# Kernel optimization log

Measured on AMD Instinct MI355X. Metric: run time of the kernel, lower is better.

The kernel has to match this reference:

```python
import jax, jax.numpy as jnp
import numpy as np

FORGET_BIAS = 1.0  # tf.nn.rnn_cell.LSTMCell default


def _lstm_scan(x_btE, W, b, hidden):
    """x: (B,T,E). W: (E+H, 4H), gate order i, j, f, o (TF LSTMCell)."""
    B = x_btE.shape[0]
    h0 = jnp.zeros((B, hidden), x_btE.dtype)
    c0 = jnp.zeros((B, hidden), x_btE.dtype)

    def step(carry, x_t):
        h, c = carry
        z = jnp.concatenate([x_t, h], axis=-1) @ W + b  # (B, 4H)
        i, j, f, o = jnp.split(z, 4, axis=-1)
        c_new = jax.nn.sigmoid(f + FORGET_BIAS) * c + jax.nn.sigmoid(i) * jnp.tanh(j)
        h_new = jax.nn.sigmoid(o) * jnp.tanh(c_new)
        return (h_new, c_new), h_new

    (_, _), hs = jax.lax.scan(step, (h0, c0), jnp.swapaxes(x_btE, 0, 1))
    return jnp.swapaxes(hs, 0, 1)  # (B, T, H)


def setup_inputs() -> dict:
    key = jax.random.key(0)
    ks = jax.random.split(key, 5)
    B, T, V, E, H, C = 256, 120, 50000, 256, 1024, 5
    tokens = jax.random.randint(ks[0], (B, T, 1), 0, V, dtype=jnp.int32)
    embeddings = jax.random.normal(ks[1], (V, E), jnp.float32) * 0.1
    W_lstm = jax.random.normal(ks[2], (E + H, 4 * H), jnp.float32) * (1.0 / np.sqrt(E + H))
    b_lstm = jnp.zeros((4 * H,), jnp.float32)
    U = jax.random.normal(ks[3], (H, C), jnp.float32) * (1.0 / np.sqrt(H))
    b2 = jnp.zeros((C,), jnp.float32)
    return {"tokens": tokens, "embeddings": embeddings, "W_lstm": W_lstm,
            "b_lstm": b_lstm, "U": U, "b2": b2}


def reference(tokens, embeddings, W_lstm, b_lstm, U, b2):
    B, T, F = tokens.shape  # F == n_features == 1
    E = embeddings.shape[1]
    H = U.shape[0]
    # embedding lookup + reshape to (B, T, F*E)
    x = embeddings[tokens].reshape(B, T, F * E)
    outputs = _lstm_scan(x, W_lstm, b_lstm, H)  # (B, T, H); dropout keep_prob=1 -> identity
    preds = outputs.reshape(-1, H) @ U + b2
    return preds.reshape(B, T, -1)  # (B, max_length, n_classes)
```

## Files before the change

### kernel.cpp

```cpp
#include <hip/hip_runtime.h>

typedef unsigned short u16;
typedef unsigned int u32;
typedef unsigned long long u64;
typedef int   v4i  __attribute__((ext_vector_type(4)));
typedef short v8s  __attribute__((ext_vector_type(8)));
typedef float v2f  __attribute__((ext_vector_type(2)));
typedef float v16f __attribute__((ext_vector_type(16)));

#define B_ 256
#define T_ 120
#define E_ 256
#define H_ 1024
#define K_ 1280
#define LDH 1032
#define LDX 264

#define WS_WF   0
#define WS_X    10485760
#define WS_HS   26214400
#define WS_BAR  89128960

__device__ __forceinline__ u16 f2bf(float f) {
    union { float f; u32 u; } v; v.f = f;
    u32 r = v.u + 0x7fffu + ((v.u >> 16) & 1u);
    return (u16)(r >> 16);
}
__device__ __forceinline__ float bf2f(u16 u) {
    union { u32 u; float f; } v; v.u = ((u32)u) << 16; return v.f;
}
__device__ __forceinline__ float fsig(float x) {
    float t = __builtin_amdgcn_exp2f(-1.44269504f * x);
    return __builtin_amdgcn_rcpf(1.0f + t);
}
__device__ __forceinline__ float ftanh_(float x) {
    float xc = fminf(8.0f, fmaxf(-8.0f, x));
    float t = __builtin_amdgcn_exp2f(2.88539008f * xc);
    return (t - 1.0f) * __builtin_amdgcn_rcpf(t + 1.0f);
}
__device__ __forceinline__ void gl_lds16(const void* g, void* l) {
    __builtin_amdgcn_global_load_lds(
        (const __attribute__((address_space(1))) void*)g,
        (__attribute__((address_space(3))) void*)l, 16, 0, 0);
}

__global__ void prep_all(const float* __restrict__ W, u16* __restrict__ Wf,
                         const int* __restrict__ tokens, const float* __restrict__ emb,
                         u16* __restrict__ X) {
    __shared__ u16 tile[64 * 72];
    int bid = blockIdx.x;
    int tid = threadIdx.x;
    if (bid < 1280) {
        int cid = bid / 5, fo = bid % 5;
        int kq  = cid & 3, np = (cid >> 2) & 1, nc = cid >> 3;
        int cc = tid & 31, n = (tid >> 5) & 1, r = tid >> 6;
        int col = (np * 2 + n) * 1024 + nc * 32 + cc;
#pragma unroll
        for (int fl = 0; fl < 4; ++fl) {
            int k0 = (4 * (fo * 4 + fl) + kq) * 16;
#pragma unroll
            for (int rr = 0; rr < 4; ++rr) {
                int krow = rr * 4 + r;
                float v = W[(size_t)(k0 + krow) * 4096 + col];
                tile[(n * 32 + cc) * 72 + fl * 16 + krow] = f2bf(v);
            }
        }
        __syncthreads();
        int lane = tid & 63, wvv = tid >> 6;
#pragma unroll
        for (int pass = 0; pass < 2; ++pass) {
            int slot = wvv + pass * 4;
            int fl = slot >> 1, nn = slot & 1;
            v4i o = *(const v4i*)&tile[(nn * 32 + (lane & 31)) * 72 + fl * 16 + ((lane >> 5) << 3)];
            *(v4i*)(Wf + (size_t)cid * 20480 + (((fo * 4 + fl) * 2 + nn) << 9) + lane * 8) = o;
        }
    } else {
        int v   = (bid - 1280) * 256 + tid;
        int e8  = v & 31;
        int row = v >> 5;
        int t = row >> 8, b = row & 255;
        int tok = tokens[b * T_ + t];
        const float* src = emb + (size_t)tok * E_ + e8 * 8;
        u16 o[8];
#pragma unroll
        for (int j = 0; j < 8; ++j) o[j] = f2bf(src[j]);
        *(v4i*)(X + (size_t)row * E_ + e8 * 8) = *(v4i*)o;
    }
}

__global__ __launch_bounds__(512, 2) void lstm_main(
    const u16* __restrict__ Wf, const u16* __restrict__ X,
    const float* __restrict__ b_lstm, u16* __restrict__ hs,
    u32* __restrict__ bar) {

    __shared__ u16  hbuf[32 * LDH];
    __shared__ u16  xbuf[32 * LDX];
    __shared__ float gates[4 * 4 * 32 * 34];
    __shared__ float bias[128];

    const int tid   = threadIdx.x;
    const int lane  = tid & 63;
    const int wv    = tid >> 6;
    const int np    = wv >> 2;
    const int kq    = wv & 3;
    const int bid   = blockIdx.x;
    const int mchunk = bid & 7;
    const int nc    = bid >> 3;
    const int m0    = mchunk << 5;

    if (tid < 128) bias[tid] = b_lstm[(tid >> 5) * H_ + (nc << 5) + (tid & 31)];

    v8s Wr[20][2];
    {
        const v4i* wsrc = (const v4i*)(Wf + (size_t)(nc * 8 + np * 4 + kq) * 20480);
#pragma unroll
        for (int f = 0; f < 20; ++f)
#pragma unroll
            for (int n = 0; n < 2; ++n)
                Wr[f][n] = __builtin_bit_cast(v8s, wsrc[(f * 2 + n) * 64 + lane]);
    }
#pragma unroll
    for (int f = 0; f < 20; ++f) {
        asm volatile("" : "+v"(Wr[f][0]));
        asm volatile("" : "+v"(Wr[f][1]));
    }

    {
        const v4i* xs = (const v4i*)(X + (size_t)m0 * E_);
#pragma unroll
        for (int i = 0; i < 2; ++i) {
            int idx = tid + i * 512;
            int r = idx >> 5, c8 = idx & 31;
            *(v4i*)&xbuf[r * LDX + c8 * 8] = xs[r * 32 + c8];
        }
    }
    __syncthreads();

    const u16* Ax = &xbuf[(lane & 31) * LDX + ((lane >> 5) << 3)];
    const u16* Ah = &hbuf[(lane & 31) * LDH + ((lane >> 5) << 3)];

    v16f acc0 = {0,0,0,0,0,0,0,0,0,0,0,0,0,0,0,0};
    v16f acc1 = {0,0,0,0,0,0,0,0,0,0,0,0,0,0,0,0};
#pragma unroll
    for (int f = 0; f < 4; ++f) {
        v8s a = *(const v8s*)(Ax + (4 * f + kq) * 16);
        acc0 = __builtin_amdgcn_mfma_f32_32x32x16_bf16(a, Wr[f][0], acc0, 0, 0, 0);
        acc1 = __builtin_amdgcn_mfma_f32_32x32x16_bf16(a, Wr[f][1], acc1, 0, 0, 0);
    }

    float cst[2] = {0.f, 0.f};
    const int cm  = tid >> 4;
    const int cn2 = (tid & 15) << 1;
    u32* hs32 = (u32*)hs;

    for (int t = 0; t < T_; ++t) {
        if (t > 0) {
            if (tid == 0) {
                u32* p = &bar[((size_t)(mchunk * T_ + (t - 1))) << 4];
                while (__hip_atomic_load(p, __ATOMIC_RELAXED, __HIP_MEMORY_SCOPE_AGENT) < 32u)
                    __builtin_amdgcn_s_sleep(1);
            }
            __syncthreads();
            {
                const u16* srcb = hs + ((size_t)(t - 1) * B_ + m0) * H_;
                const int r0 = wv << 2;
#pragma unroll
                for (int i = 0; i < 4; ++i)
                    gl_lds16(srcb + (size_t)(r0 + i) * H_ + lane * 8,
                             &hbuf[(r0 + i) * LDH]);
#pragma unroll
                for (int i = 0; i < 4; ++i)
                    gl_lds16(srcb + (size_t)(r0 + i) * H_ + 512 + lane * 8,
                             &hbuf[(r0 + i) * LDH + 512]);
            }
            asm volatile("s_waitcnt vmcnt(4)\n\ts_barrier" ::: "memory");
#pragma unroll
            for (int f = 4; f < 12; ++f) {
                v8s a = *(const v8s*)(Ah + (4 * f + kq) * 16 - 256);
                acc0 = __builtin_amdgcn_mfma_f32_32x32x16_bf16(a, Wr[f][0], acc0, 0, 0, 0);
                acc1 = __builtin_amdgcn_mfma_f32_32x32x16_bf16(a, Wr[f][1], acc1, 0, 0, 0);
            }
            asm volatile("s_waitcnt vmcnt(0)\n\ts_barrier" ::: "memory");
#pragma unroll
            for (int f = 12; f < 20; ++f) {
                v8s a = *(const v8s*)(Ah + (4 * f + kq) * 16 - 256);
                acc0 = __builtin_amdgcn_mfma_f32_32x32x16_bf16(a, Wr[f][0], acc0, 0, 0, 0);
                acc1 = __builtin_amdgcn_mfma_f32_32x32x16_bf16(a, Wr[f][1], acc1, 0, 0, 0);
            }
        }

        {
            int col = lane & 31, rq = (lane >> 5) << 2;
            float* g0 = &gates[(kq * 4 + np * 2 + 0) * 1088];
            float* g1 = &gates[(kq * 4 + np * 2 + 1) * 1088];
#pragma unroll
            for (int reg = 0; reg < 16; ++reg) {
                int row = (reg & 3) + ((reg >> 2) << 3) + rq;
                g0[row * 34 + col] = acc0[reg];
                g1[row * 34 + col] = acc1[reg];
            }
        }
        __syncthreads();

        if (t + 1 < T_) {
            const v4i* xs = (const v4i*)(X + ((size_t)(t + 1) * B_ + m0) * E_);
#pragma unroll
            for (int i = 0; i < 2; ++i) {
                int idx = tid + i * 512;
                int r = idx >> 5, c8 = idx & 31;
                *(v4i*)&xbuf[r * LDX + c8 * 8] = xs[r * 32 + c8];
            }
        }

        u32 hpack = 0;
        {
            v2f zz[4];
#pragma unroll
            for (int gg = 0; gg < 4; ++gg) {
                v2f s0 = *(const v2f*)&gates[(0 * 4 + gg) * 1088 + cm * 34 + cn2];
                v2f s1 = *(const v2f*)&gates[(1 * 4 + gg) * 1088 + cm * 34 + cn2];
                v2f s2 = *(const v2f*)&gates[(2 * 4 + gg) * 1088 + cm * 34 + cn2];
                v2f s3 = *(const v2f*)&gates[(3 * 4 + gg) * 1088 + cm * 34 + cn2];
                zz[gg].x = (s0.x + s1.x) + (s2.x + s3.x);
                zz[gg].y = (s0.y + s1.y) + (s2.y + s3.y);
            }
#pragma unroll
            for (int q = 0; q < 2; ++q) {
                int n = cn2 + q;
                float ip = zz[0][q] + bias[n];
                float jp = zz[1][q] + bias[32 + n];
                float fp = zz[2][q] + bias[64 + n] + 1.0f;
                float op = zz[3][q] + bias[96 + n];
                float cc = fsig(fp) * cst[q] + fsig(ip) * ftanh_(jp);
                cst[q] = cc;
                hpack |= ((u32)f2bf(fsig(op) * ftanh_(cc))) << (16 * q);
            }
        }
        __hip_atomic_store(&hs32[((size_t)t * B_ + m0 + cm) * 512 + (nc << 4) + (tid & 15)],
                           hpack, __ATOMIC_RELAXED, __HIP_MEMORY_SCOPE_AGENT);

        if (t + 1 < T_) {
            asm volatile("s_waitcnt vmcnt(0)" ::: "memory");
            __syncthreads();
            if (tid == 0)
                __hip_atomic_fetch_add(&bar[((size_t)(mchunk * T_ + t)) << 4], 1u,
                                       __ATOMIC_RELAXED, __HIP_MEMORY_SCOPE_AGENT);
#pragma unroll
            for (int reg = 0; reg < 16; ++reg) { acc0[reg] = 0.f; acc1[reg] = 0.f; }
#pragma unroll
            for (int f = 0; f < 4; ++f) {
                v8s a = *(const v8s*)(Ax + (4 * f + kq) * 16);
                acc0 = __builtin_amdgcn_mfma_f32_32x32x16_bf16(a, Wr[f][0], acc0, 0, 0, 0);
                acc1 = __builtin_amdgcn_mfma_f32_32x32x16_bf16(a, Wr[f][1], acc1, 0, 0, 0);
            }
        }
    }
}

__global__ void proj_kernel(const u16* __restrict__ hs, const float* __restrict__ U,
                            const float* __restrict__ b2, float* __restrict__ out) {
    __shared__ float Ul[H_ * 5];
    int tid = threadIdx.x;
    for (int i = tid; i < H_ * 5; i += 256) Ul[i] = U[i];
    __syncthreads();
    int wv = tid >> 6, lane = tid & 63;
#pragma unroll 1
    for (int i = 0; i < 16; ++i) {
        int row = blockIdx.x * 64 + wv * 16 + i;
        int t = row >> 8, b = row & 255;
        const v4i* hp = (const v4i*)(hs + (size_t)row * H_);
        float p[5] = {0.f, 0.f, 0.f, 0.f, 0.f};
#pragma unroll
        for (int half = 0; half < 2; ++half) {
            v4i hv = hp[lane * 2 + half];
            u16 us[8];
            *(v4i*)us = hv;
#pragma unroll
            for (int j = 0; j < 8; ++j) {
                float hf = bf2f(us[j]);
                int k = lane * 16 + half * 8 + j;
#pragma unroll
                for (int c = 0; c < 5; ++c) p[c] += hf * Ul[k * 5 + c];
            }
        }
#pragma unroll
        for (int c = 0; c < 5; ++c)
            for (int off = 32; off > 0; off >>= 1)
                p[c] += __shfl_down(p[c], off, 64);
        if (lane == 0) {
#pragma unroll
            for (int c = 0; c < 5; ++c)
                out[((size_t)b * T_ + t) * 5 + c] = p[c] + b2[c];
        }
    }
}

extern "C" void kernel_launch(void* const* d_in, const int* in_sizes, int n_in,
                              void* d_out, int out_size, void* d_ws, size_t ws_size,
                              hipStream_t stream) {
    const int*   tokens = (const int*)d_in[0];
    const float* emb    = (const float*)d_in[1];
    const float* W      = (const float*)d_in[2];
    const float* b_l    = (const float*)d_in[3];
    const float* U      = (const float*)d_in[4];
    const float* b2     = (const float*)d_in[5];
    float* out = (float*)d_out;

    char* ws = (char*)d_ws;
    u16* Wf  = (u16*)(ws + WS_WF);
    u16* X   = (u16*)(ws + WS_X);
    u16* hs  = (u16*)(ws + WS_HS);
    u32* bar = (u32*)(ws + WS_BAR);

    hipMemsetAsync(bar, 0, 8 * T_ * 16 * sizeof(u32), stream);
    prep_all<<<5120, 256, 0, stream>>>(W, Wf, tokens, emb, X);
    lstm_main<<<256, 512, 0, stream>>>(Wf, X, b_l, hs, bar);
    proj_kernel<<<480, 256, 0, stream>>>(hs, U, b2, out);
}
```

Baseline: 654.8 us.

## Split batch chunk into two half-tiles with 16x16 MFMA and staggered barriers

Each block's 32-row batch chunk is split into two 16-row halves processed in sequence with 16x16x32 MFMAs. Each half has its own cross-block barrier, so one half's h-load and compute can overlap the other half's gate math and barrier wait. The K reduction drops from a 4-way split to a 2-way split across waves, with each wave owning one gate, which halves the LDS gate-reduction work. The cost is more barriers per timestep and only half the threads active during the elementwise phase.

```diff
diff --git a/kernel.cpp b/kernel.cpp
--- a/kernel.cpp
+++ b/kernel.cpp
@@ -6,13 +6,12 @@
 typedef int   v4i  __attribute__((ext_vector_type(4)));
 typedef short v8s  __attribute__((ext_vector_type(8)));
 typedef float v2f  __attribute__((ext_vector_type(2)));
-typedef float v16f __attribute__((ext_vector_type(16)));
+typedef float v4f  __attribute__((ext_vector_type(4)));
 
 #define B_ 256
 #define T_ 120
 #define E_ 256
 #define H_ 1024
-#define K_ 1280
 #define LDH 1032
 #define LDX 264
 
@@ -47,32 +46,32 @@
 __global__ void prep_all(const float* __restrict__ W, u16* __restrict__ Wf,
                          const int* __restrict__ tokens, const float* __restrict__ emb,
                          u16* __restrict__ X) {
-    __shared__ u16 tile[64 * 72];
+    __shared__ u16 tile[32 * 136];
     int bid = blockIdx.x;
     int tid = threadIdx.x;
     if (bid < 1280) {
         int cid = bid / 5, fo = bid % 5;
-        int kq  = cid & 3, np = (cid >> 2) & 1, nc = cid >> 3;
-        int cc = tid & 31, n = (tid >> 5) & 1, r = tid >> 6;
-        int col = (np * 2 + n) * 1024 + nc * 32 + cc;
+        int kh = cid & 1, g = (cid >> 1) & 3, nc = cid >> 3;
+        int colbase = g * 1024 + nc * 32;
+        int cc = tid & 31, rr = tid >> 5;
 #pragma unroll
         for (int fl = 0; fl < 4; ++fl) {
-            int k0 = (4 * (fo * 4 + fl) + kq) * 16;
-#pragma unroll
-            for (int rr = 0; rr < 4; ++rr) {
-                int krow = rr * 4 + r;
-                float v = W[(size_t)(k0 + krow) * 4096 + col];
-                tile[(n * 32 + cc) * 72 + fl * 16 + krow] = f2bf(v);
+            int k0 = 32 * (2 * (fo * 4 + fl) + kh);
+#pragma unroll
+            for (int q = 0; q < 4; ++q) {
+                int krow = rr + q * 8;
+                float v = W[(size_t)(k0 + krow) * 4096 + colbase + cc];
+                tile[cc * 136 + fl * 32 + krow] = f2bf(v);
             }
         }
         __syncthreads();
         int lane = tid & 63, wvv = tid >> 6;
 #pragma unroll
         for (int pass = 0; pass < 2; ++pass) {
-            int slot = wvv + pass * 4;
-            int fl = slot >> 1, nn = slot & 1;
-            v4i o = *(const v4i*)&tile[(nn * 32 + (lane & 31)) * 72 + fl * 16 + ((lane >> 5) << 3)];
-            *(v4i*)(Wf + (size_t)cid * 20480 + (((fo * 4 + fl) * 2 + nn) << 9) + lane * 8) = o;
+            int u = wvv + pass * 4;
+            int fl = u >> 1, n = u & 1;
+            v4i o = *(const v4i*)&tile[(n * 16 + (lane & 15)) * 136 + fl * 32 + ((lane >> 4) << 3)];
+            *(v4i*)(Wf + (size_t)cid * 20480 + ((size_t)((fo * 4 + fl) * 2 + n) << 9) + lane * 8) = o;
         }
     } else {
         int v   = (bid - 1280) * 256 + tid;
@@ -93,16 +92,16 @@
     const float* __restrict__ b_lstm, u16* __restrict__ hs,
     u32* __restrict__ bar) {
 
-    __shared__ u16  hbuf[32 * LDH];
+    __shared__ u16  hbuf[2][16 * LDH];
     __shared__ u16  xbuf[32 * LDX];
-    __shared__ float gates[4 * 4 * 32 * 34];
+    __shared__ float gates[8 * 544];
     __shared__ float bias[128];
 
     const int tid   = threadIdx.x;
     const int lane  = tid & 63;
     const int wv    = tid >> 6;
-    const int np    = wv >> 2;
-    const int kq    = wv & 3;
+    const int g     = wv >> 1;
+    const int kh    = wv & 1;
     const int bid   = blockIdx.x;
     const int mchunk = bid & 7;
     const int nc    = bid >> 3;
@@ -112,7 +111,7 @@
 
     v8s Wr[20][2];
     {
-        const v4i* wsrc = (const v4i*)(Wf + (size_t)(nc * 8 + np * 4 + kq) * 20480);
+        const v4i* wsrc = (const v4i*)(Wf + (size_t)(nc * 8 + g * 2 + kh) * 20480);
 #pragma unroll
         for (int f = 0; f < 20; ++f)
 #pragma unroll
@@ -136,94 +135,69 @@
     }
     __syncthreads();
 
-    const u16* Ax = &xbuf[(lane & 31) * LDX + ((lane >> 5) << 3)];
-    const u16* Ah = &hbuf[(lane & 31) * LDH + ((lane >> 5) << 3)];
-
-    v16f acc0 = {0,0,0,0,0,0,0,0,0,0,0,0,0,0,0,0};
-    v16f acc1 = {0,0,0,0,0,0,0,0,0,0,0,0,0,0,0,0};
-#pragma unroll
-    for (int f = 0; f < 4; ++f) {
-        v8s a = *(const v8s*)(Ax + (4 * f + kq) * 16);
-        acc0 = __builtin_amdgcn_mfma_f32_32x32x16_bf16(a, Wr[f][0], acc0, 0, 0, 0);
-        acc1 = __builtin_amdgcn_mfma_f32_32x32x16_bf16(a, Wr[f][1], acc1, 0, 0, 0);
-    }
-
-    float cst[2] = {0.f, 0.f};
+    const int arow = lane & 15, aq = (lane >> 4) << 3;
+    const u16* Ax0 = &xbuf[arow * LDX + aq];
+    const u16* Ax1 = &xbuf[(16 + arow) * LDX + aq];
+    const u16* Ah0 = &hbuf[0][arow * LDH + aq];
+    const u16* Ah1 = &hbuf[1][arow * LDH + aq];
+
+    float cstA[2] = {0.f, 0.f}, cstB[2] = {0.f, 0.f};
     const int cm  = tid >> 4;
     const int cn2 = (tid & 15) << 1;
+    const int gcol = lane & 15, gr4 = (lane >> 4) << 2;
     u32* hs32 = (u32*)hs;
 
     for (int t = 0; t < T_; ++t) {
         if (t > 0) {
             if (tid == 0) {
-                u32* p = &bar[((size_t)(mchunk * T_ + (t - 1))) << 4];
+                u32* p = &bar[((size_t)((mchunk * 2 + 1) * T_ + (t - 1))) << 4];
                 while (__hip_atomic_load(p, __ATOMIC_RELAXED, __HIP_MEMORY_SCOPE_AGENT) < 32u)
                     __builtin_amdgcn_s_sleep(1);
             }
             __syncthreads();
-            {
-                const u16* srcb = hs + ((size_t)(t - 1) * B_ + m0) * H_;
-                const int r0 = wv << 2;
-#pragma unroll
-                for (int i = 0; i < 4; ++i)
-                    gl_lds16(srcb + (size_t)(r0 + i) * H_ + lane * 8,
-                             &hbuf[(r0 + i) * LDH]);
-#pragma unroll
-                for (int i = 0; i < 4; ++i)
-                    gl_lds16(srcb + (size_t)(r0 + i) * H_ + 512 + lane * 8,
-                             &hbuf[(r0 + i) * LDH + 512]);
-            }
-            asm volatile("s_waitcnt vmcnt(4)\n\ts_barrier" ::: "memory");
-#pragma unroll
-            for (int f = 4; f < 12; ++f) {
-                v8s a = *(const v8s*)(Ah + (4 * f + kq) * 16 - 256);
-                acc0 = __builtin_amdgcn_mfma_f32_32x32x16_bf16(a, Wr[f][0], acc0, 0, 0, 0);
-                acc1 = __builtin_amdgcn_mfma_f32_32x32x16_bf16(a, Wr[f][1], acc1, 0, 0, 0);
-            }
-            asm volatile("s_waitcnt vmcnt(0)\n\ts_barrier" ::: "memory");
-#pragma unroll
-            for (int f = 12; f < 20; ++f) {
-                v8s a = *(const v8s*)(Ah + (4 * f + kq) * 16 - 256);
-                acc0 = __builtin_amdgcn_mfma_f32_32x32x16_bf16(a, Wr[f][0], acc0, 0, 0, 0);
-                acc1 = __builtin_amdgcn_mfma_f32_32x32x16_bf16(a, Wr[f][1], acc1, 0, 0, 0);
-            }
-        }
-
+            const u16* src = hs + ((size_t)(t - 1) * B_ + m0 + 16) * H_;
+#pragma unroll
+            for (int i = 0; i < 4; ++i) {
+                int idx = wv * 4 + i, r = idx >> 1, hf = idx & 1;
+                gl_lds16(src + (size_t)r * H_ + hf * 512 + lane * 8,
+                         &hbuf[1][r * LDH + hf * 512]);
+            }
+        }
+
+        v4f a0 = {0,0,0,0}, a1 = {0,0,0,0};
+#pragma unroll
+        for (int f = 0; f < 4; ++f) {
+            v8s a = *(const v8s*)(Ax0 + (2 * f + kh) * 32);
+            a0 = __builtin_amdgcn_mfma_f32_16x16x32_bf16(a, Wr[f][0], a0, 0, 0, 0);
+            a1 = __builtin_amdgcn_mfma_f32_16x16x32_bf16(a, Wr[f][1], a1, 0, 0, 0);
+        }
+        if (t > 0) {
+#pragma unroll
+            for (int f = 4; f < 20; ++f) {
+                v8s a = *(const v8s*)(Ah0 + (64 * f + 32 * kh - 256));
+                a0 = __builtin_amdgcn_mfma_f32_16x16x32_bf16(a, Wr[f][0], a0, 0, 0, 0);
+                a1 = __builtin_amdgcn_mfma_f32_16x16x32_bf16(a, Wr[f][1], a1, 0, 0, 0);
+            }
+        }
         {
-            int col = lane & 31, rq = (lane >> 5) << 2;
-            float* g0 = &gates[(kq * 4 + np * 2 + 0) * 1088];
-            float* g1 = &gates[(kq * 4 + np * 2 + 1) * 1088];
-#pragma unroll
-            for (int reg = 0; reg < 16; ++reg) {
-                int row = (reg & 3) + ((reg >> 2) << 3) + rq;
-                g0[row * 34 + col] = acc0[reg];
-                g1[row * 34 + col] = acc1[reg];
-            }
-        }
-        __syncthreads();
-
-        if (t + 1 < T_) {
-            const v4i* xs = (const v4i*)(X + ((size_t)(t + 1) * B_ + m0) * E_);
-#pragma unroll
-            for (int i = 0; i < 2; ++i) {
-                int idx = tid + i * 512;
-                int r = idx >> 5, c8 = idx & 31;
-                *(v4i*)&xbuf[r * LDX + c8 * 8] = xs[r * 32 + c8];
-            }
-        }
-
-        u32 hpack = 0;
-        {
+            float* gb = &gates[(kh * 4 + g) * 544];
+#pragma unroll
+            for (int reg = 0; reg < 4; ++reg) {
+                int row = gr4 + reg;
+                gb[row * 34 + gcol]      = a0[reg];
+                gb[row * 34 + 16 + gcol] = a1[reg];
+            }
+        }
+        __syncthreads();
+        if (tid < 256) {
             v2f zz[4];
 #pragma unroll
             for (int gg = 0; gg < 4; ++gg) {
-                v2f s0 = *(const v2f*)&gates[(0 * 4 + gg) * 1088 + cm * 34 + cn2];
-                v2f s1 = *(const v2f*)&gates[(1 * 4 + gg) * 1088 + cm * 34 + cn2];
-                v2f s2 = *(const v2f*)&gates[(2 * 4 + gg) * 1088 + cm * 34 + cn2];
-                v2f s3 = *(const v2f*)&gates[(3 * 4 + gg) * 1088 + cm * 34 + cn2];
-                zz[gg].x = (s0.x + s1.x) + (s2.x + s3.x);
-                zz[gg].y = (s0.y + s1.y) + (s2.y + s3.y);
-            }
+                v2f s0 = *(const v2f*)&gates[(0 + gg) * 544 + cm * 34 + cn2];
+                v2f s1 = *(const v2f*)&gates[(4 + gg) * 544 + cm * 34 + cn2];
+                zz[gg].x = s0.x + s1.x; zz[gg].y = s0.y + s1.y;
+            }
+            u32 hpack = 0;
 #pragma unroll
             for (int q = 0; q < 2; ++q) {
                 int n = cn2 + q;
@@ -231,29 +205,94 @@
                 float jp = zz[1][q] + bias[32 + n];
                 float fp = zz[2][q] + bias[64 + n] + 1.0f;
                 float op = zz[3][q] + bias[96 + n];
-                float cc = fsig(fp) * cst[q] + fsig(ip) * ftanh_(jp);
-                cst[q] = cc;
+                float cc = fsig(fp) * cstA[q] + fsig(ip) * ftanh_(jp);
+                cstA[q] = cc;
                 hpack |= ((u32)f2bf(fsig(op) * ftanh_(cc))) << (16 * q);
             }
-        }
-        __hip_atomic_store(&hs32[((size_t)t * B_ + m0 + cm) * 512 + (nc << 4) + (tid & 15)],
-                           hpack, __ATOMIC_RELAXED, __HIP_MEMORY_SCOPE_AGENT);
-
+            __hip_atomic_store(&hs32[((size_t)t * B_ + m0 + cm) * 512 + (nc << 4) + (tid & 15)],
+                               hpack, __ATOMIC_RELAXED, __HIP_MEMORY_SCOPE_AGENT);
+        }
+        asm volatile("s_waitcnt vmcnt(0)" ::: "memory");
+        __syncthreads();
         if (t + 1 < T_) {
-            asm volatile("s_waitcnt vmcnt(0)" ::: "memory");
+            if (tid == 0) {
+                u32* p = &bar[((size_t)((mchunk * 2 + 0) * T_ + t)) << 4];
+                __hip_atomic_fetch_add(p, 1u, __ATOMIC_RELAXED, __HIP_MEMORY_SCOPE_AGENT);
+                while (__hip_atomic_load(p, __ATOMIC_RELAXED, __HIP_MEMORY_SCOPE_AGENT) < 32u)
+                    __builtin_amdgcn_s_sleep(1);
+            }
             __syncthreads();
-            if (tid == 0)
-                __hip_atomic_fetch_add(&bar[((size_t)(mchunk * T_ + t)) << 4], 1u,
-                                       __ATOMIC_RELAXED, __HIP_MEMORY_SCOPE_AGENT);
-#pragma unroll
-            for (int reg = 0; reg < 16; ++reg) { acc0[reg] = 0.f; acc1[reg] = 0.f; }
-#pragma unroll
-            for (int f = 0; f < 4; ++f) {
-                v8s a = *(const v8s*)(Ax + (4 * f + kq) * 16);
-                acc0 = __builtin_amdgcn_mfma_f32_32x32x16_bf16(a, Wr[f][0], acc0, 0, 0, 0);
-                acc1 = __builtin_amdgcn_mfma_f32_32x32x16_bf16(a, Wr[f][1], acc1, 0, 0, 0);
-            }
-        }
+            const u16* src = hs + ((size_t)t * B_ + m0) * H_;
+#pragma unroll
+            for (int i = 0; i < 4; ++i) {
+                int idx = wv * 4 + i, r = idx >> 1, hf = idx & 1;
+                gl_lds16(src + (size_t)r * H_ + hf * 512 + lane * 8,
+                         &hbuf[0][r * LDH + hf * 512]);
+            }
+        }
+
+        v4f b0 = {0,0,0,0}, b1 = {0,0,0,0};
+#pragma unroll
+        for (int f = 0; f < 4; ++f) {
+            v8s a = *(const v8s*)(Ax1 + (2 * f + kh) * 32);
+            b0 = __builtin_amdgcn_mfma_f32_16x16x32_bf16(a, Wr[f][0], b0, 0, 0, 0);
+            b1 = __builtin_amdgcn_mfma_f32_16x16x32_bf16(a, Wr[f][1], b1, 0, 0, 0);
+        }
+        if (t > 0) {
+#pragma unroll
+            for (int f = 4; f < 20; ++f) {
+                v8s a = *(const v8s*)(Ah1 + (64 * f + 32 * kh - 256));
+                b0 = __builtin_amdgcn_mfma_f32_16x16x32_bf16(a, Wr[f][0], b0, 0, 0, 0);
+                b1 = __builtin_amdgcn_mfma_f32_16x16x32_bf16(a, Wr[f][1], b1, 0, 0, 0);
+            }
+        }
+        {
+            float* gb = &gates[(kh * 4 + g) * 544];
+#pragma unroll
+            for (int reg = 0; reg < 4; ++reg) {
+                int row = gr4 + reg;
+                gb[row * 34 + gcol]      = b0[reg];
+                gb[row * 34 + 16 + gcol] = b1[reg];
+            }
+        }
+        __syncthreads();
+        if (t + 1 < T_) {
+            const v4i* xs = (const v4i*)(X + ((size_t)(t + 1) * B_ + m0) * E_);
+#pragma unroll
+            for (int i = 0; i < 2; ++i) {
+                int idx = tid + i * 512;
+                int r = idx >> 5, c8 = idx & 31;
+                *(v4i*)&xbuf[r * LDX + c8 * 8] = xs[r * 32 + c8];
+            }
+        }
+        if (tid < 256) {
+            v2f zz[4];
+#pragma unroll
+            for (int gg = 0; gg < 4; ++gg) {
+                v2f s0 = *(const v2f*)&gates[(0 + gg) * 544 + cm * 34 + cn2];
+                v2f s1 = *(const v2f*)&gates[(4 + gg) * 544 + cm * 34 + cn2];
+                zz[gg].x = s0.x + s1.x; zz[gg].y = s0.y + s1.y;
+            }
+            u32 hpack = 0;
+#pragma unroll
+            for (int q = 0; q < 2; ++q) {
+                int n = cn2 + q;
+                float ip = zz[0][q] + bias[n];
+                float jp = zz[1][q] + bias[32 + n];
+                float fp = zz[2][q] + bias[64 + n] + 1.0f;
+                float op = zz[3][q] + bias[96 + n];
+                float cc = fsig(fp) * cstB[q] + fsig(ip) * ftanh_(jp);
+                cstB[q] = cc;
+                hpack |= ((u32)f2bf(fsig(op) * ftanh_(cc))) << (16 * q);
+            }
+            __hip_atomic_store(&hs32[((size_t)t * B_ + m0 + 16 + cm) * 512 + (nc << 4) + (tid & 15)],
+                               hpack, __ATOMIC_RELAXED, __HIP_MEMORY_SCOPE_AGENT);
+        }
+        asm volatile("s_waitcnt vmcnt(0)" ::: "memory");
+        __syncthreads();
+        if (t + 1 < T_ && tid == 0)
+            __hip_atomic_fetch_add(&bar[((size_t)((mchunk * 2 + 1) * T_ + t)) << 4], 1u,
+                                   __ATOMIC_RELAXED, __HIP_MEMORY_SCOPE_AGENT);
     }
 }
 
@@ -312,7 +351,7 @@
     u16* hs  = (u16*)(ws + WS_HS);
     u32* bar = (u32*)(ws + WS_BAR);
 
-    hipMemsetAsync(bar, 0, 8 * T_ * 16 * sizeof(u32), stream);
+    hipMemsetAsync(bar, 0, 16 * T_ * 16 * sizeof(u32), stream);
     prep_all<<<5120, 256, 0, stream>>>(W, Wf, tokens, emb, X);
     lstm_main<<<256, 512, 0, stream>>>(Wf, X, b_l, hs, bar);
     proj_kernel<<<480, 256, 0, stream>>>(hs, U, b2, out);
```

Result: slower. 764.1 us (+16.7%).
